# Optimization experiments

Measured on AMD Instinct MI355X. Metric: run time of the kernel, lower is better.

Reference implementation:

```python
import jax, jax.numpy as jnp
import numpy as np

NHEAD = 16


def setup_inputs() -> dict:
    key = jax.random.key(0)
    ks = jax.random.split(key, 8)
    B, T, C = 2, 1024, 2048
    H, D = NHEAD, C // NHEAD
    P = 1024  # past kv length
    s = 0.02
    return {
        "x": jax.random.normal(ks[0], (B, T, C), jnp.float32),
        "past_k": jax.random.normal(ks[1], (B, H, P, D), jnp.float32),
        "past_v": jax.random.normal(ks[2], (B, H, P, D), jnp.float32),
        "Wk": jax.random.normal(ks[3], (C, C), jnp.float32) * s,
        "Wq": jax.random.normal(ks[4], (C, C), jnp.float32) * s,
        "Wv": jax.random.normal(ks[5], (C, C), jnp.float32) * s,
        "Wp": jax.random.normal(ks[6], (C, C), jnp.float32) * s,
        "bp": jax.random.normal(ks[7], (C,), jnp.float32) * s,
    }


def reference(x, past_k, past_v, Wk, Wq, Wv, Wp, bp):
    B, T, C = x.shape
    H = NHEAD
    D = C // H
    # nn.Linear(W): y = x @ W.T ; split into heads -> [B,H,T,D]
    def proj_heads(W):
        return (x @ W.T).reshape(B, T, H, D).transpose(0, 2, 1, 3)
    q = proj_heads(Wq)
    k_new = proj_heads(Wk)
    v_new = proj_heads(Wv)
    k = jnp.concatenate([past_k, k_new], axis=2)  # [B,H,P+T,D]
    v = jnp.concatenate([past_v, v_new], axis=2)
    past_len = past_k.shape[2]
    total_len = past_len + T
    # causal mask: new-query row i attends to absolute position j <= past_len + i
    q_pos = past_len + jnp.arange(T)[:, None]        # [T,1]
    k_pos = jnp.arange(total_len)[None, :]           # [1,total]
    mask = k_pos <= q_pos                            # [T,total]
    att = jnp.einsum("bhqd,bhkd->bhqk", q, k) * (1.0 / np.sqrt(D).astype(np.float32))
    att = jnp.where(mask[None, None], att, jnp.float32(-jnp.inf))
    att = jax.nn.softmax(att, axis=-1)
    out = jnp.einsum("bhqk,bhkd->bhqd", att, v)
    out = out.transpose(0, 2, 1, 3).reshape(B, T, C)
    out = out @ Wp.T + bp
    return out, k, v
```

## Files before the change

### kernel.cpp

```cpp
#include <hip/hip_runtime.h>
#include <stdint.h>

#define B_ 2
#define T_ 1024
#define C_ 2048
#define H_ 16
#define D_ 128
#define P_ 1024
#define L_ 2048
#define M_ 2048

typedef unsigned short u16;
typedef __attribute__((ext_vector_type(8))) short short8;
typedef __attribute__((ext_vector_type(4))) float f32x4;
typedef __attribute__((ext_vector_type(8))) u16 u16x8;
typedef __attribute__((ext_vector_type(4))) u16 u16x4;

__device__ __forceinline__ u16 f2bf(float x) {
    union { float f; uint32_t u; } c; c.f = x;
    uint32_t u = c.u;
    return (u16)((u + 0x7fffu + ((u >> 16) & 1u)) >> 16);
}

__device__ __forceinline__ void gload_lds16(const void* g, void* l) {
    typedef __attribute__((address_space(1))) const void gvoid;
    typedef __attribute__((address_space(3))) void lvoid;
    __builtin_amdgcn_global_load_lds((gvoid*)g, (lvoid*)l, 16, 0, 0);
}

__global__ __launch_bounds__(256) void prep_kernel(
        const float* __restrict__ x,  const float* __restrict__ wk,
        const float* __restrict__ wv, const float* __restrict__ wq,
        const float* __restrict__ wp,
        const float4* __restrict__ pk, const float4* __restrict__ pv,
        u16* __restrict__ xb, u16* __restrict__ obK,
        u16* __restrict__ obV, u16* __restrict__ obQ, u16* __restrict__ obP,
        float4* __restrict__ kdst, float4* __restrict__ vdst,
        u16x4* __restrict__ kb, u16* __restrict__ vbT) {
    __shared__ float s[64][65];
    const int bid = blockIdx.x;
    const int tid = threadIdx.x;
    if (bid < 8192) {
        const int r = bid >> 11;
        const int i = (bid & 2047) * 256 + tid;
        const float* src = (r == 0) ? x : (r == 1) ? wk : (r == 2) ? wv : wq;
        u16* dst = (r == 0) ? xb : (r == 1) ? obK : (r == 2) ? obV : obQ;
        float4 a = ((const float4*)src)[i * 2], b = ((const float4*)src)[i * 2 + 1];
        ((u16x8*)dst)[i] = u16x8{f2bf(a.x), f2bf(a.y), f2bf(a.z), f2bf(a.w),
                                 f2bf(b.x), f2bf(b.y), f2bf(b.z), f2bf(b.w)};
    } else if (bid < 12288) {
        const int i = (bid - 8192) * 256 + tid;
        const int bh = i >> 15;
        const int rest = i & 32767;
        const size_t dst = (size_t)bh * (L_ * D_ / 4) + rest;
        float4 k4 = pk[i], v4 = pv[i];
        kdst[dst] = k4;
        vdst[dst] = v4;
        kb[dst] = u16x4{f2bf(k4.x), f2bf(k4.y), f2bf(k4.z), f2bf(k4.w)};
    } else if (bid < 13312) {
        const int tb = bid - 12288;
        const int bh = tb >> 5;
        const int tile = tb & 31;
        const int k0 = (tile >> 1) * 64;
        const int d0 = (tile & 1) * 64;
        const float* src = (const float*)pv + ((size_t)bh * P_ + k0) * D_ + d0;
        {
            int r = tid >> 2, c0 = (tid & 3) * 16;
#pragma unroll
            for (int u = 0; u < 4; ++u) {
                float4 f = *(const float4*)(src + (size_t)r * D_ + c0 + u * 4);
                s[r][c0 + u * 4 + 0] = f.x; s[r][c0 + u * 4 + 1] = f.y;
                s[r][c0 + u * 4 + 2] = f.z; s[r][c0 + u * 4 + 3] = f.w;
            }
        }
        __syncthreads();
        int d = tid >> 2, ck = (tid & 3) * 16;
        u16* dst = vbT + ((size_t)bh * D_ + d0 + d) * L_ + k0 + ck;
        u16x8 o0, o1;
#pragma unroll
        for (int j = 0; j < 8; ++j) o0[j] = f2bf(s[ck + j][d]);
#pragma unroll
        for (int j = 0; j < 8; ++j) o1[j] = f2bf(s[ck + 8 + j][d]);
        *(u16x8*)dst = o0;
        *(u16x8*)(dst + 8) = o1;
    } else {
        const int i = (bid - 13312) * 256 + tid;
        float4 a = ((const float4*)wp)[i * 2], b = ((const float4*)wp)[i * 2 + 1];
        ((u16x8*)obP)[i] = u16x8{f2bf(a.x), f2bf(a.y), f2bf(a.z), f2bf(a.w),
                                 f2bf(b.x), f2bf(b.y), f2bf(b.z), f2bf(b.w)};
    }
}

__global__ __launch_bounds__(256) void convert_bf16_kernel(
        const float* __restrict__ in, u16* __restrict__ out) {
    int i = blockIdx.x * 256 + threadIdx.x;
    const float4* p = (const float4*)in;
    float4 a = p[i * 2], b = p[i * 2 + 1];
    ((u16x8*)out)[i] = u16x8{f2bf(a.x), f2bf(a.y), f2bf(a.z), f2bf(a.w),
                             f2bf(b.x), f2bf(b.y), f2bf(b.z), f2bf(b.w)};
}


__global__ __launch_bounds__(256) void gemm_qkv(
        const u16* __restrict__ A,
        const u16* __restrict__ wbK, const u16* __restrict__ wbV,
        const u16* __restrict__ wbQ,
        float* __restrict__ kout, float* __restrict__ vout,
        u16* __restrict__ kb, u16* __restrict__ vbT, u16* __restrict__ Qst) {
    __shared__ u16 As[3][128 * 32];
    __shared__ u16 Bs[3][128 * 32];
    const int tid  = threadIdx.x;
    const int wave = tid >> 6;
    const int lane = tid & 63;
    const int m0   = blockIdx.y * 128;
    const int n0g  = blockIdx.x * 128;
    const int region = n0g >> 11;
    const int n0   = n0g & 2047;
    const u16* Bw = (region == 0) ? wbK : (region == 1) ? wbV : wbQ;

    f32x4 acc[4][4];
#pragma unroll
    for (int i = 0; i < 4; ++i)
#pragma unroll
        for (int j = 0; j < 4; ++j) acc[i][j] = f32x4{0.f, 0.f, 0.f, 0.f};

    const int srow = lane >> 2;
    const int scol = (lane & 3) * 8;
    const int q0 = wave * 2, q1 = wave * 2 + 1;
    const u16* A0 = A  + (size_t)(m0 + q0 * 16 + srow) * C_ + scol;
    const u16* A1 = A  + (size_t)(m0 + q1 * 16 + srow) * C_ + scol;
    const u16* B0 = Bw + (size_t)(n0 + q0 * 16 + srow) * C_ + scol;
    const u16* B1 = Bw + (size_t)(n0 + q1 * 16 + srow) * C_ + scol;

    const int frow = lane & 15;
    const int fko  = (lane >> 4) * 8;
    const int wr = (wave >> 1) * 64;
    const int wc = (wave & 1) * 64;

    u16 *Ac = &As[0][0], *An = &As[1][0], *Af = &As[2][0];
    u16 *Bc = &Bs[0][0], *Bn = &Bs[1][0], *Bf = &Bs[2][0];

    gload_lds16(A0,      Ac + q0 * 512);
    gload_lds16(A1,      Ac + q1 * 512);
    gload_lds16(B0,      Bc + q0 * 512);
    gload_lds16(B1,      Bc + q1 * 512);
    gload_lds16(A0 + 32, An + q0 * 512);
    gload_lds16(A1 + 32, An + q1 * 512);
    gload_lds16(B0 + 32, Bn + q0 * 512);
    gload_lds16(B1 + 32, Bn + q1 * 512);

    for (int kt = 0; kt < C_ - 32; kt += 32) {
        asm volatile("s_waitcnt vmcnt(4)" ::: "memory");
        __builtin_amdgcn_s_barrier();
        asm volatile("" ::: "memory");
        if (kt + 64 < C_) {
            gload_lds16(A0 + kt + 64, Af + q0 * 512);
            gload_lds16(A1 + kt + 64, Af + q1 * 512);
            gload_lds16(B0 + kt + 64, Bf + q0 * 512);
            gload_lds16(B1 + kt + 64, Bf + q1 * 512);
        }
        short8 af[4], bf[4];
#pragma unroll
        for (int i = 0; i < 4; ++i) {
            af[i] = *(const short8*)&Ac[(wr + i * 16 + frow) * 32 + fko];
            bf[i] = *(const short8*)&Bc[(wc + i * 16 + frow) * 32 + fko];
        }
#pragma unroll
        for (int mi = 0; mi < 4; ++mi)
#pragma unroll
            for (int ni = 0; ni < 4; ++ni)
                acc[mi][ni] = __builtin_amdgcn_mfma_f32_16x16x32_bf16(
                    af[mi], bf[ni], acc[mi][ni], 0, 0, 0);
        u16* t;
        t = Ac; Ac = An; An = Af; Af = t;
        t = Bc; Bc = Bn; Bn = Bf; Bf = t;
    }
    {
        asm volatile("s_waitcnt vmcnt(0)" ::: "memory");
        __builtin_amdgcn_s_barrier();
        asm volatile("" ::: "memory");
        short8 af[4], bf[4];
#pragma unroll
        for (int i = 0; i < 4; ++i) {
            af[i] = *(const short8*)&Ac[(wr + i * 16 + frow) * 32 + fko];
            bf[i] = *(const short8*)&Bc[(wc + i * 16 + frow) * 32 + fko];
        }
#pragma unroll
        for (int mi = 0; mi < 4; ++mi)
#pragma unroll
            for (int ni = 0; ni < 4; ++ni)
                acc[mi][ni] = __builtin_amdgcn_mfma_f32_16x16x32_bf16(
                    af[mi], bf[ni], acc[mi][ni], 0, 0, 0);
    }

    const int ccol = lane & 15;
    const int crb  = (lane >> 4) * 4;
#pragma unroll
    for (int mi = 0; mi < 4; ++mi) {
#pragma unroll
        for (int ni = 0; ni < 4; ++ni) {
            const int gc  = n0 + wc + ni * 16 + ccol;
            const int grb = m0 + wr + mi * 16 + crb;
            if (region == 2) {
#pragma unroll
                for (int r = 0; r < 4; ++r)
                    Qst[(size_t)(grb + r) * C_ + gc] = f2bf(acc[mi][ni][r]);
            } else {
                const int b = grb >> 10, tb = grb & 1023;
                const int h = gc >> 7,  d  = gc & 127;
                const size_t fb = (((size_t)(b * H_ + h)) * L_ + P_ + tb) * D_ + d;
                if (region == 0) {
#pragma unroll
                    for (int r = 0; r < 4; ++r) {
                        kout[fb + (size_t)r * D_] = acc[mi][ni][r];
                        kb[fb + (size_t)r * D_]   = f2bf(acc[mi][ni][r]);
                    }
                } else {
#pragma unroll
                    for (int r = 0; r < 4; ++r) vout[fb + (size_t)r * D_] = acc[mi][ni][r];
                    const size_t tb2 = (((size_t)(b * H_ + h)) * D_ + d) * L_ + P_ + tb;
                    *(u16x4*)&vbT[tb2] = u16x4{
                        f2bf(acc[mi][ni][0]), f2bf(acc[mi][ni][1]),
                        f2bf(acc[mi][ni][2]), f2bf(acc[mi][ni][3])};
                }
            }
        }
    }
}

template <int MODE>
__global__ __launch_bounds__(256) void gemm128(
        const u16* __restrict__ A, const u16* __restrict__ Bw,
        float* __restrict__ outf, u16* __restrict__ outb,
        const float* __restrict__ bias) {
    __shared__ u16 As[3][128 * 32];
    __shared__ u16 Bs[3][128 * 32];
    const int tid  = threadIdx.x;
    const int wave = tid >> 6;
    const int lane = tid & 63;
    const int m0 = blockIdx.y * 128;
    const int n0 = blockIdx.x * 128;

    f32x4 acc[4][4];
#pragma unroll
    for (int i = 0; i < 4; ++i)
#pragma unroll
        for (int j = 0; j < 4; ++j) acc[i][j] = f32x4{0.f, 0.f, 0.f, 0.f};

    const int srow = lane >> 2;
    const int scol = (lane & 3) * 8;
    const int q0 = wave * 2, q1 = wave * 2 + 1;
    const u16* A0 = A  + (size_t)(m0 + q0 * 16 + srow) * C_ + scol;
    const u16* A1 = A  + (size_t)(m0 + q1 * 16 + srow) * C_ + scol;
    const u16* B0 = Bw + (size_t)(n0 + q0 * 16 + srow) * C_ + scol;
    const u16* B1 = Bw + (size_t)(n0 + q1 * 16 + srow) * C_ + scol;

    const int frow = lane & 15;
    const int fko  = (lane >> 4) * 8;
    const int wr = (wave >> 1) * 64;
    const int wc = (wave & 1) * 64;

    u16 *Ac = &As[0][0], *An = &As[1][0], *Af = &As[2][0];
    u16 *Bc = &Bs[0][0], *Bn = &Bs[1][0], *Bf = &Bs[2][0];

    gload_lds16(A0,      Ac + q0 * 512);
    gload_lds16(A1,      Ac + q1 * 512);
    gload_lds16(B0,      Bc + q0 * 512);
    gload_lds16(B1,      Bc + q1 * 512);
    gload_lds16(A0 + 32, An + q0 * 512);
    gload_lds16(A1 + 32, An + q1 * 512);
    gload_lds16(B0 + 32, Bn + q0 * 512);
    gload_lds16(B1 + 32, Bn + q1 * 512);

    for (int kt = 0; kt < C_ - 32; kt += 32) {
        asm volatile("s_waitcnt vmcnt(4)" ::: "memory");
        __builtin_amdgcn_s_barrier();
        asm volatile("" ::: "memory");
        if (kt + 64 < C_) {
            gload_lds16(A0 + kt + 64, Af + q0 * 512);
            gload_lds16(A1 + kt + 64, Af + q1 * 512);
            gload_lds16(B0 + kt + 64, Bf + q0 * 512);
            gload_lds16(B1 + kt + 64, Bf + q1 * 512);
        }
        short8 af[4], bf[4];
#pragma unroll
        for (int i = 0; i < 4; ++i) {
            af[i] = *(const short8*)&Ac[(wr + i * 16 + frow) * 32 + fko];
            bf[i] = *(const short8*)&Bc[(wc + i * 16 + frow) * 32 + fko];
        }
#pragma unroll
        for (int mi = 0; mi < 4; ++mi)
#pragma unroll
            for (int ni = 0; ni < 4; ++ni)
                acc[mi][ni] = __builtin_amdgcn_mfma_f32_16x16x32_bf16(
                    af[mi], bf[ni], acc[mi][ni], 0, 0, 0);
        u16* t;
        t = Ac; Ac = An; An = Af; Af = t;
        t = Bc; Bc = Bn; Bn = Bf; Bf = t;
    }
    {
        asm volatile("s_waitcnt vmcnt(0)" ::: "memory");
        __builtin_amdgcn_s_barrier();
        asm volatile("" ::: "memory");
        short8 af[4], bf[4];
#pragma unroll
        for (int i = 0; i < 4; ++i) {
            af[i] = *(const short8*)&Ac[(wr + i * 16 + frow) * 32 + fko];
            bf[i] = *(const short8*)&Bc[(wc + i * 16 + frow) * 32 + fko];
        }
#pragma unroll
        for (int mi = 0; mi < 4; ++mi)
#pragma unroll
            for (int ni = 0; ni < 4; ++ni)
                acc[mi][ni] = __builtin_amdgcn_mfma_f32_16x16x32_bf16(
                    af[mi], bf[ni], acc[mi][ni], 0, 0, 0);
    }

    const int ccol = lane & 15;
    const int crb  = (lane >> 4) * 4;
#pragma unroll
    for (int mi = 0; mi < 4; ++mi) {
#pragma unroll
        for (int ni = 0; ni < 4; ++ni) {
            const int gc  = n0 + wc + ni * 16 + ccol;
            const int grb = m0 + wr + mi * 16 + crb;
            if (MODE == 0) {
#pragma unroll
                for (int r = 0; r < 4; ++r)
                    outb[(size_t)(grb + r) * C_ + gc] = f2bf(acc[mi][ni][r]);
            } else {
                const float ba = bias[gc];
#pragma unroll
                for (int r = 0; r < 4; ++r)
                    outf[(size_t)(grb + r) * C_ + gc] = acc[mi][ni][r] + ba;
            }
        }
    }
}

#define NEG_BIG -30000.f
__global__ __launch_bounds__(256) void attn_kernel(
        const u16* __restrict__ Q, const u16* __restrict__ Kb,
        const u16* __restrict__ VT, u16* __restrict__ O) {
    __shared__ u16 Qs[64 * 128];
    __shared__ u16 Ks[64 * 128];
    __shared__ u16 Vs[128 * 64];
    __shared__ u16 Ps[64][72];

    const int tid  = threadIdx.x;
    const int wave = tid >> 6;
    const int lane = tid & 63;
    int       qt = blockIdx.x & 15;
    const int h  = (blockIdx.x >> 4) & 15;
    const int b  = blockIdx.x >> 8;
    if (b) qt = 15 - qt;
    const int t0 = qt * 64;

    const u16* Kbase = Kb + (size_t)(b * H_ + h) * L_ * D_;
    const u16* Vbase = VT + (size_t)(b * H_ + h) * D_ * L_;

#pragma unroll
    for (int i = 0; i < 4; ++i) {
        int g   = (wave * 4 + i) * 64 + lane;
        int row = g >> 4, blk = g & 15;
        int sb  = (blk & 8) | ((blk ^ row) & 7);
        gload_lds16(Q + ((size_t)(b * T_ + t0 + row)) * C_ + h * D_ + sb * 8,
                    &Qs[(wave * 4 + i) * 512]);
    }

    const int frow = lane & 15;
    const int quad = lane >> 4;
    const int fko  = quad * 8;
    const int swz  = (frow & 7) << 3;

    f32x4 o_acc[8];
#pragma unroll
    for (int n = 0; n < 8; ++n) o_acc[n] = f32x4{0.f, 0.f, 0.f, 0.f};
    float m_i[4] = {NEG_BIG, NEG_BIG, NEG_BIG, NEG_BIG};
    float l_i[4] = {0.f, 0.f, 0.f, 0.f};
    const float scale = 0.08838834764831845f;

    const int nch = (P_ + t0 + 64) >> 6;
    const int wave_lim = P_ + t0 + wave * 16 + 15;

    for (int ch = 0; ch < nch; ++ch) {
        const int j0 = ch * 64;
        __syncthreads();
#pragma unroll
        for (int i = 0; i < 4; ++i) {
            int g = (wave * 4 + i) * 64 + lane;
            {
                int row = g >> 4, blk = g & 15;
                int sb  = (blk & 8) | ((blk ^ row) & 7);
                gload_lds16(Kbase + (size_t)(j0 + row) * D_ + sb * 8,
                            &Ks[(wave * 4 + i) * 512]);
            }
            {
                int d  = g >> 3, cb = g & 7;
                int sb = (cb ^ d) & 7;
                gload_lds16(Vbase + (size_t)d * L_ + j0 + sb * 8,
                            &Vs[(wave * 4 + i) * 512]);
            }
        }
        __syncthreads();

        const bool active = (j0 <= wave_lim);

        if (active) {
            f32x4 st[4];
#pragma unroll
            for (int j = 0; j < 4; ++j) st[j] = f32x4{0.f, 0.f, 0.f, 0.f};
            __builtin_amdgcn_s_setprio(1);
#pragma unroll
            for (int kt = 0; kt < 4; ++kt) {
                short8 a = *(const short8*)&Qs[(wave * 16 + frow) * 128 +
                                               ((kt * 32 + fko) ^ swz)];
#pragma unroll
                for (int j = 0; j < 4; ++j) {
                    short8 kf = *(const short8*)&Ks[(j * 16 + frow) * 128 +
                                                    ((kt * 32 + fko) ^ swz)];
                    st[j] = __builtin_amdgcn_mfma_f32_16x16x32_bf16(a, kf, st[j], 0, 0, 0);
                }
            }
            __builtin_amdgcn_s_setprio(0);

#pragma unroll
            for (int r = 0; r < 4; ++r) {
                const int t   = t0 + wave * 16 + quad * 4 + r;
                const int lim = P_ + t;
                float sv[4];
                float mx = NEG_BIG;
#pragma unroll
                for (int j = 0; j < 4; ++j) {
                    int jg = j0 + j * 16 + frow;
                    float s = st[j][r] * scale;
                    s = (jg <= lim) ? s : NEG_BIG;
                    sv[j] = s;
                    mx = fmaxf(mx, s);
                }
#pragma unroll
                for (int sft = 1; sft <= 8; sft <<= 1)
                    mx = fmaxf(mx, __shfl_xor(mx, sft, 64));
                float m_new = fmaxf(m_i[r], mx);
                float alpha = __expf(fminf(m_i[r] - m_new, 0.f));
                float rs = 0.f;
#pragma unroll
                for (int j = 0; j < 4; ++j) {
                    float p = __expf(fminf(sv[j] - m_new, 0.f));
                    p = (sv[j] <= NEG_BIG) ? 0.f : p;
                    sv[j] = p;
                    rs += p;
                }
#pragma unroll
                for (int sft = 1; sft <= 8; sft <<= 1)
                    rs += __shfl_xor(rs, sft, 64);
                l_i[r] = l_i[r] * alpha + rs;
                m_i[r] = m_new;
#pragma unroll
                for (int n = 0; n < 8; ++n) o_acc[n][r] *= alpha;
#pragma unroll
                for (int j = 0; j < 4; ++j)
                    Ps[wave * 16 + quad * 4 + r][j * 16 + frow] = f2bf(sv[j]);
            }
        }
        __syncthreads();

        if (active) {
            __builtin_amdgcn_s_setprio(1);
#pragma unroll
            for (int kt2 = 0; kt2 < 2; ++kt2) {
                short8 a = *(const short8*)&Ps[wave * 16 + frow][kt2 * 32 + fko];
#pragma unroll
                for (int n = 0; n < 8; ++n) {
                    short8 vf = *(const short8*)&Vs[(n * 16 + frow) * 64 +
                                                    ((kt2 * 32 + fko) ^ swz)];
                    o_acc[n] = __builtin_amdgcn_mfma_f32_16x16x32_bf16(a, vf, o_acc[n], 0, 0, 0);
                }
            }
            __builtin_amdgcn_s_setprio(0);
        }
    }

#pragma unroll
    for (int r = 0; r < 4; ++r) {
        float rl = 1.f / fmaxf(l_i[r], 1e-30f);
        int t = t0 + wave * 16 + quad * 4 + r;
#pragma unroll
        for (int n = 0; n < 8; ++n) {
            float v = o_acc[n][r] * rl;
            O[((size_t)(b * T_ + t)) * C_ + h * D_ + n * 16 + frow] = f2bf(v);
        }
    }
}

extern "C" void kernel_launch(void* const* d_in, const int* in_sizes, int n_in,
                              void* d_out, int out_size, void* d_ws, size_t ws_size,
                              hipStream_t stream) {
    const float* x      = (const float*)d_in[0];
    const float* past_k = (const float*)d_in[1];
    const float* past_v = (const float*)d_in[2];
    const float* Wk     = (const float*)d_in[3];
    const float* Wq     = (const float*)d_in[4];
    const float* Wv     = (const float*)d_in[5];
    const float* Wp     = (const float*)d_in[6];
    const float* bp     = (const float*)d_in[7];

    float* out  = (float*)d_out;
    float* kout = out + 4194304;
    float* vout = kout + 8388608;

    u16* Qst = (u16*)d_out;
    u16* xb  = (u16*)((char*)d_out + (8u << 20));
    u16* OstWq = (u16*)d_ws;
    u16* kb    = (u16*)((char*)d_ws + (8u  << 20));
    u16* vbT   = (u16*)((char*)d_ws + (24u << 20));
    u16* wbKP  = (u16*)((char*)d_ws + (40u << 20));
    const bool fused = ws_size >= (size_t)(56u << 20);
    const bool bigws = ws_size >= (size_t)(64u << 20);
    u16* wbV = fused ? (u16*)((char*)d_ws + (48u << 20))
                     : Qst;
    u16* wbP = bigws ? (u16*)((char*)d_ws + (56u << 20)) : wbKP;

    prep_kernel<<<bigws ? 15360 : 13312, 256, 0, stream>>>(
        x, Wk, Wv, Wq, Wp,
        (const float4*)past_k, (const float4*)past_v,
        xb, wbKP, wbV, OstWq, bigws ? wbP : nullptr,
        (float4*)kout, (float4*)vout, (u16x4*)kb, vbT);

    if (fused) {
        dim3 g(48, 16);
        gemm_qkv<<<g, 256, 0, stream>>>(xb, wbKP, wbV, OstWq,
                                        kout, vout, kb, vbT, Qst);
    } else {
        dim3 gkv(32, 16);
        gemm_qkv<<<gkv, 256, 0, stream>>>(xb, wbKP, wbV, OstWq,
                                          kout, vout, kb, vbT, Qst);
        dim3 gq(16, 16);
        gemm128<0><<<gq, 256, 0, stream>>>(xb, OstWq, nullptr, Qst, nullptr);
    }

    attn_kernel<<<512, 256, 0, stream>>>(Qst, kb, vbT, OstWq);

    if (!bigws) convert_bf16_kernel<<<2048, 256, 0, stream>>>(Wp, wbKP);
    dim3 gp(16, 16);
    gemm128<2><<<gp, 256, 0, stream>>>(OstWq, wbP, out, nullptr, bp);
}
```

Before: 386.3 us.

## Prefetch next K/V chunk into registers and skip masking on full tiles

In the attention kernel, the direct global-to-LDS loads are replaced by register-staged prefetching. The next 64-key chunk of K and V is loaded into registers while the current chunk is computed, then written to LDS after a raw s_barrier. This is meant to hide global load latency behind the MFMA and softmax work. It also skips the causal mask compare on chunks fully below the diagonal and drops the clamp and zero-select around exp. The hand-placed waitcnt and barrier sequence adds register pressure and ordering risk. Without the zero-select, correctness depends on NEG_BIG underflowing exp to zero.

```diff
diff --git a/kernel.cpp b/kernel.cpp
--- a/kernel.cpp
+++ b/kernel.cpp
@@ -100,7 +100,6 @@
                              f2bf(b.x), f2bf(b.y), f2bf(b.z), f2bf(b.w)};
 }
 
-
 __global__ __launch_bounds__(256) void gemm_qkv(
         const u16* __restrict__ A,
         const u16* __restrict__ wbK, const u16* __restrict__ wbV,
@@ -368,6 +367,33 @@
                     &Qs[(wave * 4 + i) * 512]);
     }
 
+    int koff[4], voff[4];
+    u16 *kdst[4], *vdst[4];
+#pragma unroll
+    for (int i = 0; i < 4; ++i) {
+        int g = (wave * 4 + i) * 64 + lane;
+        {
+            int row = g >> 4, blk = g & 15;
+            int sb  = (blk & 8) | ((blk ^ row) & 7);
+            koff[i] = row * D_ + sb * 8;
+            kdst[i] = &Ks[(wave * 4 + i) * 512 + lane * 8];
+        }
+        {
+            int d  = g >> 3, cb = g & 7;
+            int sb = (cb ^ d) & 7;
+            voff[i] = d * L_ + sb * 8;
+            vdst[i] = &Vs[(wave * 4 + i) * 512 + lane * 8];
+        }
+    }
+
+    u16x8 kreg[4], vreg[4];
+#pragma unroll
+    for (int i = 0; i < 4; ++i) {
+        kreg[i] = *(const u16x8*)(Kbase + koff[i]);
+        vreg[i] = *(const u16x8*)(Vbase + voff[i]);
+    }
+    asm volatile("s_waitcnt vmcnt(8)" ::: "memory");
+
     const int frow = lane & 15;
     const int quad = lane >> 4;
     const int fko  = quad * 8;
@@ -385,24 +411,24 @@
 
     for (int ch = 0; ch < nch; ++ch) {
         const int j0 = ch * 64;
-        __syncthreads();
-#pragma unroll
-        for (int i = 0; i < 4; ++i) {
-            int g = (wave * 4 + i) * 64 + lane;
-            {
-                int row = g >> 4, blk = g & 15;
-                int sb  = (blk & 8) | ((blk ^ row) & 7);
-                gload_lds16(Kbase + (size_t)(j0 + row) * D_ + sb * 8,
-                            &Ks[(wave * 4 + i) * 512]);
-            }
-            {
-                int d  = g >> 3, cb = g & 7;
-                int sb = (cb ^ d) & 7;
-                gload_lds16(Vbase + (size_t)d * L_ + j0 + sb * 8,
-                            &Vs[(wave * 4 + i) * 512]);
-            }
-        }
-        __syncthreads();
+        asm volatile("" ::: "memory");
+        __builtin_amdgcn_s_barrier();
+        asm volatile("" ::: "memory");
+#pragma unroll
+        for (int i = 0; i < 4; ++i) *(u16x8*)kdst[i] = kreg[i];
+#pragma unroll
+        for (int i = 0; i < 4; ++i) *(u16x8*)vdst[i] = vreg[i];
+        asm volatile("s_waitcnt lgkmcnt(0)" ::: "memory");
+        __builtin_amdgcn_s_barrier();
+        asm volatile("" ::: "memory");
+        if (ch + 1 < nch) {
+            const int jn = j0 + 64;
+#pragma unroll
+            for (int i = 0; i < 4; ++i) {
+                kreg[i] = *(const u16x8*)(Kbase + (size_t)jn * D_ + koff[i]);
+                vreg[i] = *(const u16x8*)(Vbase + jn + voff[i]);
+            }
+        }
 
         const bool active = (j0 <= wave_lim);
 
@@ -424,17 +450,19 @@
             }
             __builtin_amdgcn_s_setprio(0);
 
+            const bool full = (j0 + 63 <= P_ + t0 + wave * 16);
 #pragma unroll
             for (int r = 0; r < 4; ++r) {
-                const int t   = t0 + wave * 16 + quad * 4 + r;
-                const int lim = P_ + t;
+                const int lim = P_ + t0 + wave * 16 + quad * 4 + r;
                 float sv[4];
                 float mx = NEG_BIG;
 #pragma unroll
                 for (int j = 0; j < 4; ++j) {
-                    int jg = j0 + j * 16 + frow;
                     float s = st[j][r] * scale;
-                    s = (jg <= lim) ? s : NEG_BIG;
+                    if (!full) {
+                        int jg = j0 + j * 16 + frow;
+                        s = (jg <= lim) ? s : NEG_BIG;
+                    }
                     sv[j] = s;
                     mx = fmaxf(mx, s);
                 }
@@ -442,12 +470,11 @@
                 for (int sft = 1; sft <= 8; sft <<= 1)
                     mx = fmaxf(mx, __shfl_xor(mx, sft, 64));
                 float m_new = fmaxf(m_i[r], mx);
-                float alpha = __expf(fminf(m_i[r] - m_new, 0.f));
+                float alpha = __expf(m_i[r] - m_new);
                 float rs = 0.f;
 #pragma unroll
                 for (int j = 0; j < 4; ++j) {
-                    float p = __expf(fminf(sv[j] - m_new, 0.f));
-                    p = (sv[j] <= NEG_BIG) ? 0.f : p;
+                    float p = __expf(sv[j] - m_new);
                     sv[j] = p;
                     rs += p;
                 }
@@ -463,7 +490,9 @@
                     Ps[wave * 16 + quad * 4 + r][j * 16 + frow] = f2bf(sv[j]);
             }
         }
-        __syncthreads();
+        asm volatile("s_waitcnt lgkmcnt(0)" ::: "memory");
+        __builtin_amdgcn_s_barrier();
+        asm volatile("" ::: "memory");
 
         if (active) {
             __builtin_amdgcn_s_setprio(1);
```

Result: no change. 384.3 us (-0.5%).
